# Optimization experiments

Measured on AMD Instinct MI355X. Metric: run time of the kernel, lower is better.

The kernel has to match this reference:

```python
import jax, jax.numpy as jnp
import numpy as np

V, E, H, S = 32000, 1024, 1024, 2048


def setup_inputs() -> dict:
    key = jax.random.key(0)
    ks = jax.random.split(key, 16)
    std = 0.02
    return {
        "encoder_out": jax.random.normal(ks[0], (S, E), jnp.float32),
        "word_input": jax.random.randint(ks[1], (1,), 0, V, jnp.int32),
        "last_context": jax.random.normal(ks[2], (1, H), jnp.float32),
        "h0": jnp.zeros((1, 1, H), jnp.float32),
        "c0": jnp.zeros((1, 1, H), jnp.float32),
        # learned parameters
        "emb": jax.random.normal(ks[3], (V, E), jnp.float32) * std,
        "W_ih": jax.random.normal(ks[4], (4 * H, E + H), jnp.float32) * std,
        "W_hh": jax.random.normal(ks[5], (4 * H, H), jnp.float32) * std,
        "b_ih": jnp.zeros((4 * H,), jnp.float32),
        "b_hh": jnp.zeros((4 * H,), jnp.float32),
        "W_attn": jax.random.normal(ks[6], (H, E + H), jnp.float32) * std,
        "b_attn": jnp.zeros((H,), jnp.float32),
        "v": jax.random.uniform(ks[7], (H,), jnp.float32) * 0.1,
        "W_ah": jax.random.normal(ks[8], (H, E + H), jnp.float32) * std,
        "b_ah": jnp.zeros((H,), jnp.float32),
        "W_out": jax.random.normal(ks[9], (V, H), jnp.float32) * std,
        "b_out": jnp.zeros((V,), jnp.float32),
    }


def reference(encoder_out, word_input, last_context, h0, c0,
              emb, W_ih, W_hh, b_ih, b_hh,
              W_attn, b_attn, v, W_ah, b_ah, W_out, b_out):
    # single decoder step, batch=1 (dropout in eval mode == identity)
    embedded = emb[word_input[0]]                       # [E]
    x = jnp.concatenate([last_context[0], embedded])    # [H+E] (context first, as in torch.cat)
    # LSTM cell (PyTorch gate order i, f, g, o)
    gates = W_ih @ x + b_ih + W_hh @ h0[0, 0] + b_hh    # [4H]
    i, f, g, o = jnp.split(gates, 4)
    c = jax.nn.sigmoid(f) * c0[0, 0] + jax.nn.sigmoid(i) * jnp.tanh(g)
    ht = jax.nn.sigmoid(o) * jnp.tanh(c)                # [H]
    # additive attention, vectorized over encoder steps.
    # original concatenates (ht, encoder_out[i]); split attn weight accordingly.
    Wa_h, Wa_e = W_attn[:, :H], W_attn[:, H:]
    scores = jnp.tanh(encoder_out @ Wa_e.T + (Wa_h @ ht + b_attn)) @ v  # [S]
    w = jax.nn.softmax(scores)                          # [S]
    context = w @ encoder_out                           # [E]
    ht_tilda = jnp.tanh(W_ah @ jnp.concatenate([context, ht]) + b_ah)  # [H]
    output = jax.nn.log_softmax(W_out @ ht_tilda + b_out)              # [V]
    return (output[None, :], (ht[None, None, :], c[None, None, :]),
            ht_tilda[None, :], w[None, :])
```

## Files before the change

### kernel.cpp

```cpp
#include <hip/hip_runtime.h>
#include <math.h>

#define V_ 32000
#define E_ 1024
#define H_ 1024
#define S_ 2048

typedef __attribute__((ext_vector_type(8))) short bf16x8;
typedef __attribute__((ext_vector_type(8))) unsigned short u16x8;
typedef __attribute__((ext_vector_type(4))) float f32x4;

typedef __attribute__((address_space(1))) const unsigned int gu32;
typedef __attribute__((address_space(3))) unsigned int lu32;

__device__ __forceinline__ float sigmoidf_(float x) { return 1.0f / (1.0f + expf(-x)); }

__device__ __forceinline__ unsigned short f2bf(float f) {
    unsigned int u = __builtin_bit_cast(unsigned int, f);
    unsigned int r = (u + 0x7fffu + ((u >> 16) & 1u)) >> 16;
    return (unsigned short)r;
}
__device__ __forceinline__ float bf2f(unsigned short u) {
    return __builtin_bit_cast(float, ((unsigned int)u) << 16);
}
__device__ __forceinline__ u16x8 pack8(f32x4 a, f32x4 b) {
    u16x8 p;
    p[0] = f2bf(a[0]); p[1] = f2bf(a[1]); p[2] = f2bf(a[2]); p[3] = f2bf(a[3]);
    p[4] = f2bf(b[0]); p[5] = f2bf(b[1]); p[6] = f2bf(b[2]); p[7] = f2bf(b[3]);
    return p;
}
__device__ __forceinline__ void gload16(const void* g, void* l) {
    __builtin_amdgcn_global_load_lds((gu32*)g, (lu32*)l, 16, 0, 0);
}
__device__ __forceinline__ f32x4 ntload4(const float* p) {
    return __builtin_nontemporal_load((const f32x4*)p);
}

__global__ __launch_bounds__(256) void kA(
    const float* __restrict__ W_ih, const float* __restrict__ W_hh,
    const float* __restrict__ b_ih, const float* __restrict__ b_hh,
    const float* __restrict__ last_context, const float* __restrict__ emb,
    const int* __restrict__ word, const float* __restrict__ h0,
    const float* __restrict__ c0, const float* __restrict__ enc,
    const float* __restrict__ W_attn,
    float* __restrict__ out_ht, float* __restrict__ out_c,
    float* __restrict__ ws_ht, unsigned short* __restrict__ encb,
    unsigned short* __restrict__ wab, float* __restrict__ ws_ctx)
{
    int b = blockIdx.x, tid = threadIdx.x;
    int wave = tid >> 6, lane = tid & 63;
    if (b < 1024) {
        __shared__ float sbuf[4];
        int j = b;
        const float* embrow = emb + (size_t)word[0] * E_;
        int row = j + wave * H_;
        const float* wi = W_ih + (size_t)row * (E_ + H_);
        const float* wh = W_hh + (size_t)row * H_;
        float acc = 0.f;
        #pragma unroll
        for (int it = 0; it < 8; ++it) {
            int idx = (lane + it * 64) * 4;
            f32x4 wv = ntload4(wi + idx);
            float4 xv = (idx < H_) ? *(const float4*)(last_context + idx)
                                   : *(const float4*)(embrow + (idx - H_));
            acc = fmaf(wv[0], xv.x, acc); acc = fmaf(wv[1], xv.y, acc);
            acc = fmaf(wv[2], xv.z, acc); acc = fmaf(wv[3], xv.w, acc);
        }
        #pragma unroll
        for (int it = 0; it < 4; ++it) {
            int idx = (lane + it * 64) * 4;
            f32x4 wv = ntload4(wh + idx);
            float4 hv = *(const float4*)(h0 + idx);
            acc = fmaf(wv[0], hv.x, acc); acc = fmaf(wv[1], hv.y, acc);
            acc = fmaf(wv[2], hv.z, acc); acc = fmaf(wv[3], hv.w, acc);
        }
        #pragma unroll
        for (int m = 32; m; m >>= 1) acc += __shfl_down(acc, m, 64);
        if (lane == 0) sbuf[wave] = acc;
        __syncthreads();
        if (tid == 0) {
            float gi = sbuf[0] + b_ih[j]          + b_hh[j];
            float gf = sbuf[1] + b_ih[j + H_]     + b_hh[j + H_];
            float gg = sbuf[2] + b_ih[j + 2*H_]   + b_hh[j + 2*H_];
            float go = sbuf[3] + b_ih[j + 3*H_]   + b_hh[j + 3*H_];
            float c  = sigmoidf_(gf) * c0[j] + sigmoidf_(gi) * tanhf(gg);
            float ht = sigmoidf_(go) * tanhf(c);
            out_c[j]  = c;
            out_ht[j] = ht;
            ws_ht[j]  = ht;
        }
        if (b == 0) {
            ws_ctx[tid]       = 0.f;
            ws_ctx[tid + 256] = 0.f;
            ws_ctx[tid + 512] = 0.f;
            ws_ctx[tid + 768] = 0.f;
        }
    } else {
        int cid = (b - 1024) * 256 + tid;
        const int ENC_CH = (S_ * E_) / 8;
        #pragma unroll
        for (int i = 0; i < 3; ++i) {
            int idx = cid + i * 131072;
            const float* src;
            unsigned short* dst;
            if (idx < ENC_CH) {
                src = enc + (size_t)idx * 8;
                dst = encb + (size_t)idx * 8;
            } else {
                int w = idx - ENC_CH;
                int h = w >> 7, off = (w & 127) * 8;
                src = W_attn + (size_t)h * (E_ + H_) + H_ + off;
                dst = wab + (size_t)h * E_ + off;
            }
            f32x4 a = ntload4(src);
            f32x4 bq = ntload4(src + 4);
            *(u16x8*)dst = pack8(a, bq);
        }
    }
}

__global__ __launch_bounds__(256) void kC(
    const float* __restrict__ W_attn, const float* __restrict__ b_attn,
    const float* __restrict__ ws_ht,
    const unsigned short* __restrict__ encb, const unsigned short* __restrict__ wab,
    const float* __restrict__ v, float* __restrict__ spart)
{
    __shared__ unsigned short As[64 * 64];
    __shared__ unsigned short Bs[64 * 64];
    __shared__ float qsh[64], vsh[64];
    int bx = blockIdx.x, by = blockIdx.y;
    int s0 = bx * 64, h0 = by * 64;
    int tid = threadIdx.x;
    int wave = tid >> 6, lane = tid & 63;

    if (tid < 64) vsh[tid] = v[h0 + tid];

    int r0 = tid >> 3, p0 = tid & 7;
    int lc = (p0 ^ (r0 & 7)) * 8;
    const unsigned short* aS0 = encb + (size_t)(s0 + r0) * E_ + lc;
    const unsigned short* aS1 = encb + (size_t)(s0 + 32 + r0) * E_ + lc;
    const unsigned short* bS0 = wab  + (size_t)(h0 + r0) * E_ + lc;
    const unsigned short* bS1 = wab  + (size_t)(h0 + 32 + r0) * E_ + lc;

    int wr = (wave >> 1) * 32, wc = (wave & 1) * 32;
    int fc = lane & 15, g = lane >> 4;
    int aRow[2], bRow[2], pc[2];
    #pragma unroll
    for (int m = 0; m < 2; ++m) aRow[m] = (wr + m * 16 + fc) * 64;
    #pragma unroll
    for (int n = 0; n < 2; ++n) bRow[n] = (wc + n * 16 + fc) * 64;
    #pragma unroll
    for (int kk = 0; kk < 2; ++kk) pc[kk] = ((kk * 4 + g) ^ (fc & 7)) * 8;

    f32x4 acc[2][2];
    #pragma unroll
    for (int m = 0; m < 2; ++m)
        #pragma unroll
        for (int n = 0; n < 2; ++n)
            acc[m][n] = (f32x4){0.f, 0.f, 0.f, 0.f};

    gload16(aS0, As + tid * 8);
    gload16(aS1, As + (tid + 256) * 8);
    gload16(bS0, Bs + tid * 8);
    gload16(bS1, Bs + (tid + 256) * 8);

    #pragma unroll 1
    for (int t = 0; t < 16; ++t) {
        __syncthreads();
        #pragma unroll
        for (int kk = 0; kk < 2; ++kk) {
            bf16x8 af[2], bf2[2];
            #pragma unroll
            for (int m = 0; m < 2; ++m) af[m] = *(const bf16x8*)(As + aRow[m] + pc[kk]);
            #pragma unroll
            for (int n = 0; n < 2; ++n) bf2[n] = *(const bf16x8*)(Bs + bRow[n] + pc[kk]);
            #pragma unroll
            for (int m = 0; m < 2; ++m)
                #pragma unroll
                for (int n = 0; n < 2; ++n)
                    acc[m][n] = __builtin_amdgcn_mfma_f32_16x16x32_bf16(
                        af[m], bf2[n], acc[m][n], 0, 0, 0);
        }
        {
            int r = h0 + wave * 16 + t;
            const float* rowp = W_attn + (size_t)r * (E_ + H_);
            float qa = 0.f;
            #pragma unroll
            for (int it = 0; it < 4; ++it) {
                int idx = (lane + it * 64) * 4;
                float4 wv = *(const float4*)(rowp + idx);
                float4 hv = *(const float4*)(ws_ht + idx);
                qa = fmaf(wv.x, hv.x, qa); qa = fmaf(wv.y, hv.y, qa);
                qa = fmaf(wv.z, hv.z, qa); qa = fmaf(wv.w, hv.w, qa);
            }
            #pragma unroll
            for (int m = 32; m; m >>= 1) qa += __shfl_down(qa, m, 64);
            if (lane == 0) qsh[wave * 16 + t] = qa + b_attn[r];
        }
        __syncthreads();
        if (t < 15) {
            int k0 = (t + 1) * 64;
            gload16(aS0 + k0, As + tid * 8);
            gload16(aS1 + k0, As + (tid + 256) * 8);
            gload16(bS0 + k0, Bs + tid * 8);
            gload16(bS1 + k0, Bs + (tid + 256) * 8);
        }
    }

    float qv[2], vv[2];
    #pragma unroll
    for (int n = 0; n < 2; ++n) {
        int col = wc + n * 16 + fc;
        qv[n] = qsh[col];
        vv[n] = vsh[col];
    }
    int part = by * 2 + (wave & 1);
    #pragma unroll
    for (int m = 0; m < 2; ++m) {
        #pragma unroll
        for (int j = 0; j < 4; ++j) {
            float p = 0.f;
            #pragma unroll
            for (int n = 0; n < 2; ++n)
                p += tanhf(acc[m][n][j] + qv[n]) * vv[n];
            #pragma unroll
            for (int mask = 8; mask; mask >>= 1) p += __shfl_xor(p, mask, 64);
            if (fc == 0)
                spart[(size_t)(s0 + wr + m * 16 + g * 4 + j) * 32 + part] = p;
        }
    }
}

__global__ __launch_bounds__(256) void kD(
    const float* __restrict__ spart, const unsigned short* __restrict__ encb,
    float* __restrict__ expw, float* __restrict__ gpart, float* __restrict__ ctx)
{
    __shared__ float esh[16];
    int b = blockIdx.x, tid = threadIdx.x;
    int s0 = b * 16;
    int sl = tid >> 4, pp = tid & 15;
    float vsum = spart[(size_t)(s0 + sl) * 32 + pp]
               + spart[(size_t)(s0 + sl) * 32 + pp + 16];
    #pragma unroll
    for (int mask = 8; mask; mask >>= 1) vsum += __shfl_xor(vsum, mask, 64);
    if (pp == 0) {
        float e = expf(vsum);
        expw[s0 + sl] = e;
        esh[sl] = e;
    }
    __syncthreads();
    if (tid == 0) {
        float bs = 0.f;
        #pragma unroll
        for (int i = 0; i < 16; ++i) bs += esh[i];
        gpart[b] = bs;
    }
    int e0 = tid * 4;
    float a0 = 0.f, a1 = 0.f, a2 = 0.f, a3 = 0.f;
    #pragma unroll
    for (int ss = 0; ss < 16; ++ss) {
        ushort4 u = *(const ushort4*)(encb + (size_t)(s0 + ss) * E_ + e0);
        float w = esh[ss];
        a0 = fmaf(w, bf2f(u.x), a0);
        a1 = fmaf(w, bf2f(u.y), a1);
        a2 = fmaf(w, bf2f(u.z), a2);
        a3 = fmaf(w, bf2f(u.w), a3);
    }
    atomicAdd(&ctx[e0 + 0], a0);
    atomicAdd(&ctx[e0 + 1], a1);
    atomicAdd(&ctx[e0 + 2], a2);
    atomicAdd(&ctx[e0 + 3], a3);
}

__global__ __launch_bounds__(256) void kE(
    const float* __restrict__ W_ah, const float* __restrict__ b_ah,
    const float* __restrict__ ctx, const float* __restrict__ ht,
    const float* __restrict__ gpart, const float* __restrict__ expw,
    float* __restrict__ out_htt, float* __restrict__ ws_htt,
    float* __restrict__ out_w)
{
    int b = blockIdx.x;
    int wave = threadIdx.x >> 6, lane = threadIdx.x & 63;
    float gsum = gpart[lane] + gpart[lane + 64];
    #pragma unroll
    for (int m = 32; m; m >>= 1) gsum += __shfl_xor(gsum, m, 64);
    float invS = 1.0f / gsum;
    if (b >= 256) {
        int s = (b - 256) * 1024 + (int)threadIdx.x * 4;
        float4 e4 = *(const float4*)(expw + s);
        float4 w4 = { e4.x * invS, e4.y * invS, e4.z * invS, e4.w * invS };
        *(float4*)(out_w + s) = w4;
        return;
    }
    int r = b * 4 + wave;
    const float* row = W_ah + (size_t)r * (E_ + H_);
    float acc = 0.f;
    #pragma unroll
    for (int it = 0; it < 8; ++it) {
        int idx = (lane + it * 64) * 4;
        f32x4 wv = ntload4(row + idx);
        float4 xv;
        if (idx < E_) {
            float4 cv = *(const float4*)(ctx + idx);
            xv = (float4){ cv.x * invS, cv.y * invS, cv.z * invS, cv.w * invS };
        } else {
            xv = *(const float4*)(ht + idx - E_);
        }
        acc = fmaf(wv[0], xv.x, acc); acc = fmaf(wv[1], xv.y, acc);
        acc = fmaf(wv[2], xv.z, acc); acc = fmaf(wv[3], xv.w, acc);
    }
    #pragma unroll
    for (int m = 32; m; m >>= 1) acc += __shfl_down(acc, m, 64);
    if (lane == 0) {
        float val = tanhf(acc + b_ah[r]);
        out_htt[r] = val;
        ws_htt[r]  = val;
    }
}

__global__ __launch_bounds__(256) void kF(
    const float* __restrict__ W_out, const float* __restrict__ b_out,
    const float* __restrict__ ht_tilda, float* __restrict__ logits,
    float* __restrict__ lpart)
{
    __shared__ float wes[4];
    int b = blockIdx.x;
    int wave = threadIdx.x >> 6, lane = threadIdx.x & 63;
    int r0 = b * 16 + wave * 4;
    const float* w0 = W_out + (size_t)r0 * H_;
    const float* w1 = W_out + (size_t)(r0 + 1) * H_;
    const float* w2 = W_out + (size_t)(r0 + 2) * H_;
    const float* w3 = W_out + (size_t)(r0 + 3) * H_;
    float a0 = 0.f, a1 = 0.f, a2 = 0.f, a3 = 0.f;
    #pragma unroll
    for (int it = 0; it < 4; ++it) {
        int idx = (lane + it * 64) * 4;
        float4 hv = *(const float4*)(ht_tilda + idx);
        f32x4 v0 = ntload4(w0 + idx);
        f32x4 v1 = ntload4(w1 + idx);
        f32x4 v2 = ntload4(w2 + idx);
        f32x4 v3 = ntload4(w3 + idx);
        a0 = fmaf(v0[0], hv.x, a0); a0 = fmaf(v0[1], hv.y, a0);
        a0 = fmaf(v0[2], hv.z, a0); a0 = fmaf(v0[3], hv.w, a0);
        a1 = fmaf(v1[0], hv.x, a1); a1 = fmaf(v1[1], hv.y, a1);
        a1 = fmaf(v1[2], hv.z, a1); a1 = fmaf(v1[3], hv.w, a1);
        a2 = fmaf(v2[0], hv.x, a2); a2 = fmaf(v2[1], hv.y, a2);
        a2 = fmaf(v2[2], hv.z, a2); a2 = fmaf(v2[3], hv.w, a2);
        a3 = fmaf(v3[0], hv.x, a3); a3 = fmaf(v3[1], hv.y, a3);
        a3 = fmaf(v3[2], hv.z, a3); a3 = fmaf(v3[3], hv.w, a3);
    }
    #pragma unroll
    for (int m = 32; m; m >>= 1) {
        a0 += __shfl_down(a0, m, 64); a1 += __shfl_down(a1, m, 64);
        a2 += __shfl_down(a2, m, 64); a3 += __shfl_down(a3, m, 64);
    }
    if (lane == 0) {
        float lg0 = a0 + b_out[r0];
        float lg1 = a1 + b_out[r0 + 1];
        float lg2 = a2 + b_out[r0 + 2];
        float lg3 = a3 + b_out[r0 + 3];
        logits[r0]     = lg0;
        logits[r0 + 1] = lg1;
        logits[r0 + 2] = lg2;
        logits[r0 + 3] = lg3;
        wes[wave] = expf(lg0) + expf(lg1) + expf(lg2) + expf(lg3);
    }
    __syncthreads();
    if (threadIdx.x == 0)
        lpart[b] = wes[0] + wes[1] + wes[2] + wes[3];
}

__global__ __launch_bounds__(1024) void kG(
    float* __restrict__ out, const float* __restrict__ lpart)
{
    __shared__ float sred[16];
    int b = blockIdx.x, tid = threadIdx.x;
    float s = 0.f;
    #pragma unroll
    for (int k = 0; k < 2; ++k) {
        int i = tid + k * 1024;
        if (i < 2000) s += lpart[i];
    }
    #pragma unroll
    for (int m = 32; m; m >>= 1) s += __shfl_down(s, m, 64);
    if ((tid & 63) == 0) sred[tid >> 6] = s;
    __syncthreads();
    float tot = 0.f;
    #pragma unroll
    for (int i = 0; i < 16; ++i) tot += sred[i];
    float lse = logf(tot);
    #pragma unroll
    for (int k = 0; k < 4; ++k) {
        int row = b * 4000 + k * 1024 + tid;
        if (row < (b + 1) * 4000 && row < V_) out[row] -= lse;
    }
}

extern "C" void kernel_launch(void* const* d_in, const int* in_sizes, int n_in,
                              void* d_out, int out_size, void* d_ws, size_t ws_size,
                              hipStream_t stream) {
    const float* enc          = (const float*)d_in[0];
    const int*   word         = (const int*)  d_in[1];
    const float* last_context = (const float*)d_in[2];
    const float* h0           = (const float*)d_in[3];
    const float* c0           = (const float*)d_in[4];
    const float* emb          = (const float*)d_in[5];
    const float* W_ih         = (const float*)d_in[6];
    const float* W_hh         = (const float*)d_in[7];
    const float* b_ih         = (const float*)d_in[8];
    const float* b_hh         = (const float*)d_in[9];
    const float* W_attn       = (const float*)d_in[10];
    const float* b_attn       = (const float*)d_in[11];
    const float* v            = (const float*)d_in[12];
    const float* W_ah         = (const float*)d_in[13];
    const float* b_ah         = (const float*)d_in[14];
    const float* W_out        = (const float*)d_in[15];
    const float* b_out        = (const float*)d_in[16];

    float* out        = (float*)d_out;
    float* out_logits = out;
    float* out_ht     = out + V_;
    float* out_c      = out + V_ + H_;
    float* out_htt    = out + V_ + 2 * H_;
    float* out_w      = out + V_ + 3 * H_;

    float* ws      = (float*)d_ws;
    float* ws_ht   = ws;
    float* ws_expw = ws + 1024;
    float* ws_ctx  = ws + 3072;
    float* ws_gp   = ws + 4096;
    float* ws_htt  = ws + 4224;
    float* ws_lp   = ws + 5248;
    float* ws_sp   = ws + 16384;
    unsigned short* encb = (unsigned short*)(ws + 81920);
    unsigned short* wab  = encb + (size_t)S_ * E_;

    kA<<<1536, 256, 0, stream>>>(W_ih, W_hh, b_ih, b_hh, last_context, emb, word,
                                 h0, c0, enc, W_attn, out_ht, out_c, ws_ht,
                                 encb, wab, ws_ctx);
    kC<<<dim3(32, 16), 256, 0, stream>>>(W_attn, b_attn, ws_ht, encb, wab, v, ws_sp);
    kD<<<128, 256, 0, stream>>>(ws_sp, encb, ws_expw, ws_gp, ws_ctx);
    kE<<<258, 256, 0, stream>>>(W_ah, b_ah, ws_ctx, ws_ht, ws_gp, ws_expw,
                                out_htt, ws_htt, out_w);
    kF<<<2000, 256, 0, stream>>>(W_out, b_out, ws_htt, out_logits, ws_lp);
    kG<<<8, 1024, 0, stream>>>(out_logits, ws_lp);
}
```

Before: 92.41 us.

## Drop nontemporal loads and hoist attention query matvec out of MFMA loop

Replaces nontemporal float4 loads with ordinary cached loads in the LSTM, conversion, W_ah and W_out kernels. In the attention-score kernel, the per-tile query matvec (Wa_h @ ht) that ran one row per k-step inside the MFMA loop now runs up front. It processes four rows at a time with ht kept in registers, overlapping with the first async LDS tile load. The intent is to reduce per-iteration latency in the GEMM loop and let loads use the cache. In exchange, the query work now serializes before the MFMA loop, and cached loads may pollute L2 on large weight streams.

After: 82.20 us. 11.0% less time.

```diff
diff --git a/kernel.cpp b/kernel.cpp
--- a/kernel.cpp
+++ b/kernel.cpp
@@ -23,17 +23,14 @@
 __device__ __forceinline__ float bf2f(unsigned short u) {
     return __builtin_bit_cast(float, ((unsigned int)u) << 16);
 }
-__device__ __forceinline__ u16x8 pack8(f32x4 a, f32x4 b) {
+__device__ __forceinline__ u16x8 pack8(float4 a, float4 b) {
     u16x8 p;
-    p[0] = f2bf(a[0]); p[1] = f2bf(a[1]); p[2] = f2bf(a[2]); p[3] = f2bf(a[3]);
-    p[4] = f2bf(b[0]); p[5] = f2bf(b[1]); p[6] = f2bf(b[2]); p[7] = f2bf(b[3]);
+    p[0] = f2bf(a.x); p[1] = f2bf(a.y); p[2] = f2bf(a.z); p[3] = f2bf(a.w);
+    p[4] = f2bf(b.x); p[5] = f2bf(b.y); p[6] = f2bf(b.z); p[7] = f2bf(b.w);
     return p;
 }
 __device__ __forceinline__ void gload16(const void* g, void* l) {
     __builtin_amdgcn_global_load_lds((gu32*)g, (lu32*)l, 16, 0, 0);
-}
-__device__ __forceinline__ f32x4 ntload4(const float* p) {
-    return __builtin_nontemporal_load((const f32x4*)p);
 }
 
 __global__ __launch_bounds__(256) void kA(
@@ -60,19 +57,19 @@
         #pragma unroll
         for (int it = 0; it < 8; ++it) {
             int idx = (lane + it * 64) * 4;
-            f32x4 wv = ntload4(wi + idx);
+            float4 wv = *(const float4*)(wi + idx);
             float4 xv = (idx < H_) ? *(const float4*)(last_context + idx)
                                    : *(const float4*)(embrow + (idx - H_));
-            acc = fmaf(wv[0], xv.x, acc); acc = fmaf(wv[1], xv.y, acc);
-            acc = fmaf(wv[2], xv.z, acc); acc = fmaf(wv[3], xv.w, acc);
+            acc = fmaf(wv.x, xv.x, acc); acc = fmaf(wv.y, xv.y, acc);
+            acc = fmaf(wv.z, xv.z, acc); acc = fmaf(wv.w, xv.w, acc);
         }
         #pragma unroll
         for (int it = 0; it < 4; ++it) {
             int idx = (lane + it * 64) * 4;
-            f32x4 wv = ntload4(wh + idx);
+            float4 wv = *(const float4*)(wh + idx);
             float4 hv = *(const float4*)(h0 + idx);
-            acc = fmaf(wv[0], hv.x, acc); acc = fmaf(wv[1], hv.y, acc);
-            acc = fmaf(wv[2], hv.z, acc); acc = fmaf(wv[3], hv.w, acc);
+            acc = fmaf(wv.x, hv.x, acc); acc = fmaf(wv.y, hv.y, acc);
+            acc = fmaf(wv.z, hv.z, acc); acc = fmaf(wv.w, hv.w, acc);
         }
         #pragma unroll
         for (int m = 32; m; m >>= 1) acc += __shfl_down(acc, m, 64);
@@ -112,8 +109,8 @@
                 src = W_attn + (size_t)h * (E_ + H_) + H_ + off;
                 dst = wab + (size_t)h * E_ + off;
             }
-            f32x4 a = ntload4(src);
-            f32x4 bq = ntload4(src + 4);
+            float4 a = *(const float4*)src;
+            float4 bq = *(const float4*)(src + 4);
             *(u16x8*)dst = pack8(a, bq);
         }
     }
@@ -133,8 +130,6 @@
     int tid = threadIdx.x;
     int wave = tid >> 6, lane = tid & 63;
 
-    if (tid < 64) vsh[tid] = v[h0 + tid];
-
     int r0 = tid >> 3, p0 = tid & 7;
     int lc = (p0 ^ (r0 & 7)) * 8;
     const unsigned short* aS0 = encb + (size_t)(s0 + r0) * E_ + lc;
@@ -142,27 +137,62 @@
     const unsigned short* bS0 = wab  + (size_t)(h0 + r0) * E_ + lc;
     const unsigned short* bS1 = wab  + (size_t)(h0 + 32 + r0) * E_ + lc;
 
-    int wr = (wave >> 1) * 32, wc = (wave & 1) * 32;
-    int fc = lane & 15, g = lane >> 4;
-    int aRow[2], bRow[2], pc[2];
-    #pragma unroll
-    for (int m = 0; m < 2; ++m) aRow[m] = (wr + m * 16 + fc) * 64;
-    #pragma unroll
-    for (int n = 0; n < 2; ++n) bRow[n] = (wc + n * 16 + fc) * 64;
-    #pragma unroll
-    for (int kk = 0; kk < 2; ++kk) pc[kk] = ((kk * 4 + g) ^ (fc & 7)) * 8;
-
-    f32x4 acc[2][2];
-    #pragma unroll
-    for (int m = 0; m < 2; ++m)
-        #pragma unroll
-        for (int n = 0; n < 2; ++n)
-            acc[m][n] = (f32x4){0.f, 0.f, 0.f, 0.f};
-
     gload16(aS0, As + tid * 8);
     gload16(aS1, As + (tid + 256) * 8);
     gload16(bS0, Bs + tid * 8);
     gload16(bS1, Bs + (tid + 256) * 8);
+
+    {
+        float4 hv[4];
+        #pragma unroll
+        for (int it = 0; it < 4; ++it)
+            hv[it] = *(const float4*)(ws_ht + (lane + it * 64) * 4);
+        #pragma unroll 1
+        for (int bq = 0; bq < 4; ++bq) {
+            int rbase = h0 + wave * 16 + bq * 4;
+            float qa[4];
+            #pragma unroll
+            for (int rr = 0; rr < 4; ++rr) {
+                const float* rowp = W_attn + (size_t)(rbase + rr) * (E_ + H_);
+                float a = 0.f;
+                #pragma unroll
+                for (int it = 0; it < 4; ++it) {
+                    float4 wv = *(const float4*)(rowp + (lane + it * 64) * 4);
+                    a = fmaf(wv.x, hv[it].x, a); a = fmaf(wv.y, hv[it].y, a);
+                    a = fmaf(wv.z, hv[it].z, a); a = fmaf(wv.w, hv[it].w, a);
+                }
+                qa[rr] = a;
+            }
+            #pragma unroll
+            for (int rr = 0; rr < 4; ++rr) {
+                #pragma unroll
+                for (int m = 32; m; m >>= 1) qa[rr] += __shfl_down(qa[rr], m, 64);
+            }
+            if (lane == 0) {
+                #pragma unroll
+                for (int rr = 0; rr < 4; ++rr)
+                    qsh[wave * 16 + bq * 4 + rr] = qa[rr] + b_attn[rbase + rr];
+            }
+        }
+    }
+    if (tid < 64) vsh[tid] = v[h0 + tid];
+
+    int wr = (wave >> 1) * 32, wc = (wave & 1) * 32;
+    int fc = lane & 15, g = lane >> 4;
+    int aRow[2], bRow[2], pc[2];
+    #pragma unroll
+    for (int m = 0; m < 2; ++m) aRow[m] = (wr + m * 16 + fc) * 64;
+    #pragma unroll
+    for (int n = 0; n < 2; ++n) bRow[n] = (wc + n * 16 + fc) * 64;
+    #pragma unroll
+    for (int kk = 0; kk < 2; ++kk) pc[kk] = ((kk * 4 + g) ^ (fc & 7)) * 8;
+
+    f32x4 acc[2][2];
+    #pragma unroll
+    for (int m = 0; m < 2; ++m)
+        #pragma unroll
+        for (int n = 0; n < 2; ++n)
+            acc[m][n] = (f32x4){0.f, 0.f, 0.f, 0.f};
 
     #pragma unroll 1
     for (int t = 0; t < 16; ++t) {
@@ -180,22 +210,6 @@
                 for (int n = 0; n < 2; ++n)
                     acc[m][n] = __builtin_amdgcn_mfma_f32_16x16x32_bf16(
                         af[m], bf2[n], acc[m][n], 0, 0, 0);
-        }
-        {
-            int r = h0 + wave * 16 + t;
-            const float* rowp = W_attn + (size_t)r * (E_ + H_);
-            float qa = 0.f;
-            #pragma unroll
-            for (int it = 0; it < 4; ++it) {
-                int idx = (lane + it * 64) * 4;
-                float4 wv = *(const float4*)(rowp + idx);
-                float4 hv = *(const float4*)(ws_ht + idx);
-                qa = fmaf(wv.x, hv.x, qa); qa = fmaf(wv.y, hv.y, qa);
-                qa = fmaf(wv.z, hv.z, qa); qa = fmaf(wv.w, hv.w, qa);
-            }
-            #pragma unroll
-            for (int m = 32; m; m >>= 1) qa += __shfl_down(qa, m, 64);
-            if (lane == 0) qsh[wave * 16 + t] = qa + b_attn[r];
         }
         __syncthreads();
         if (t < 15) {
@@ -298,7 +312,7 @@
     #pragma unroll
     for (int it = 0; it < 8; ++it) {
         int idx = (lane + it * 64) * 4;
-        f32x4 wv = ntload4(row + idx);
+        float4 wv = *(const float4*)(row + idx);
         float4 xv;
         if (idx < E_) {
             float4 cv = *(const float4*)(ctx + idx);
@@ -306,8 +320,8 @@
         } else {
             xv = *(const float4*)(ht + idx - E_);
         }
-        acc = fmaf(wv[0], xv.x, acc); acc = fmaf(wv[1], xv.y, acc);
-        acc = fmaf(wv[2], xv.z, acc); acc = fmaf(wv[3], xv.w, acc);
+        acc = fmaf(wv.x, xv.x, acc); acc = fmaf(wv.y, xv.y, acc);
+        acc = fmaf(wv.z, xv.z, acc); acc = fmaf(wv.w, xv.w, acc);
     }
     #pragma unroll
     for (int m = 32; m; m >>= 1) acc += __shfl_down(acc, m, 64);
@@ -336,18 +350,18 @@
     for (int it = 0; it < 4; ++it) {
         int idx = (lane + it * 64) * 4;
         float4 hv = *(const float4*)(ht_tilda + idx);
-        f32x4 v0 = ntload4(w0 + idx);
-        f32x4 v1 = ntload4(w1 + idx);
-        f32x4 v2 = ntload4(w2 + idx);
-        f32x4 v3 = ntload4(w3 + idx);
-        a0 = fmaf(v0[0], hv.x, a0); a0 = fmaf(v0[1], hv.y, a0);
-        a0 = fmaf(v0[2], hv.z, a0); a0 = fmaf(v0[3], hv.w, a0);
-        a1 = fmaf(v1[0], hv.x, a1); a1 = fmaf(v1[1], hv.y, a1);
-        a1 = fmaf(v1[2], hv.z, a1); a1 = fmaf(v1[3], hv.w, a1);
-        a2 = fmaf(v2[0], hv.x, a2); a2 = fmaf(v2[1], hv.y, a2);
-        a2 = fmaf(v2[2], hv.z, a2); a2 = fmaf(v2[3], hv.w, a2);
-        a3 = fmaf(v3[0], hv.x, a3); a3 = fmaf(v3[1], hv.y, a3);
-        a3 = fmaf(v3[2], hv.z, a3); a3 = fmaf(v3[3], hv.w, a3);
+        float4 v0 = *(const float4*)(w0 + idx);
+        float4 v1 = *(const float4*)(w1 + idx);
+        float4 v2 = *(const float4*)(w2 + idx);
+        float4 v3 = *(const float4*)(w3 + idx);
+        a0 = fmaf(v0.x, hv.x, a0); a0 = fmaf(v0.y, hv.y, a0);
+        a0 = fmaf(v0.z, hv.z, a0); a0 = fmaf(v0.w, hv.w, a0);
+        a1 = fmaf(v1.x, hv.x, a1); a1 = fmaf(v1.y, hv.y, a1);
+        a1 = fmaf(v1.z, hv.z, a1); a1 = fmaf(v1.w, hv.w, a1);
+        a2 = fmaf(v2.x, hv.x, a2); a2 = fmaf(v2.y, hv.y, a2);
+        a2 = fmaf(v2.z, hv.z, a2); a2 = fmaf(v2.w, hv.w, a2);
+        a3 = fmaf(v3.x, hv.x, a3); a3 = fmaf(v3.y, hv.y, a3);
+        a3 = fmaf(v3.z, hv.z, a3); a3 = fmaf(v3.w, hv.w, a3);
     }
     #pragma unroll
     for (int m = 32; m; m >>= 1) {
```
